# Kernel tuning notes

Measured on AMD Instinct MI355X. Metric: run time of the kernel, lower is better.

Reference implementation:

```python
import jax, jax.numpy as jnp
import numpy as np

SQ, SK, B, H, D = 2048, 2048, 2, 16, 64
LAYER_NUMBER = 1  # coeff for query_key_layer_scaling
MASK_FILL = -10000.0  # attention_mask_func fill value


def setup_inputs() -> dict:
    key = jax.random.key(0)
    kq, kk, kv = jax.random.split(key, 3)
    query_layer = jax.random.normal(kq, (SQ, B, H, D), dtype=jnp.float32)
    key_layer = jax.random.normal(kk, (SK, B, H, D), dtype=jnp.float32)
    value_layer = jax.random.normal(kv, (SK, B, H, D), dtype=jnp.float32)
    attention_mask = jnp.zeros((B, 1, SQ, SK), dtype=bool)  # ignored for causal mask type
    return {
        "query_layer": query_layer,
        "key_layer": key_layer,
        "value_layer": value_layer,
        "attention_mask": attention_mask,
    }


def reference(query_layer, key_layer, value_layer, attention_mask):
    sq, b, h, d = query_layer.shape
    sk = key_layer.shape[0]
    coeff = float(LAYER_NUMBER)
    norm_factor = np.sqrt(d) * coeff  # norm_factor = sqrt(d) * layer_number

    # BMM1: [b,h,sq,sk] scores, scaled by 1/norm_factor
    scores = jnp.einsum("sbhd,tbhd->bhst", query_layer, key_layer) / norm_factor

    # FusedScaleMaskSoftmax: scale by coeff in fp32, causal mask, softmax
    scores = scores.astype(jnp.float32) * coeff
    causal = jnp.triu(jnp.ones((sq, sk), dtype=bool), k=1)  # True above diagonal -> masked
    scores = jnp.where(causal[None, None], MASK_FILL, scores)
    probs = jax.nn.softmax(scores, axis=-1).astype(query_layer.dtype)

    # dropout p=0.0 -> identity

    # BMM2: context [sq,b,h,d] -> [sq,b,h*d]
    context = jnp.einsum("bhst,tbhd->sbhd", probs, value_layer)
    return context.reshape(sq, b, h * d)
```

## Files before the change

kernel.cpp:

```cpp
#include <hip/hip_runtime.h>

typedef short bf16x8 __attribute__((ext_vector_type(8)));
typedef float f32x4 __attribute__((ext_vector_type(4)));
typedef unsigned u32x4 __attribute__((ext_vector_type(4)));
typedef unsigned u32x2 __attribute__((ext_vector_type(2)));
typedef unsigned short ushort_t;

#define RS 2048
#define LDSK 72
#define QSCALE 0.18033688011f
#define BH_STRIDE (2048*64)

static __device__ __forceinline__ unsigned pkbf(float a, float b) {
    union { float f; unsigned u; } ua, ub; ua.f = a; ub.f = b;
    return ((ua.u + 0x8000u) >> 16) | ((ub.u + 0x8000u) & 0xffff0000u);
}

static __device__ __forceinline__ float fexp2(float x) {
#if __has_builtin(__builtin_amdgcn_exp2f)
    return __builtin_amdgcn_exp2f(x);
#else
    return exp2f(x);
#endif
}

__global__ __launch_bounds__(256)
void prep_bf16(const float* __restrict__ K, const float* __restrict__ V,
               ushort_t* __restrict__ Kbf, ushort_t* __restrict__ Vtb)
{
    __shared__ short Tt[64 * LDSK];
    const int kt = blockIdx.x, bh = blockIdx.y;
    const int t = threadIdx.x;
    {
        const int key = t >> 2, cq = (t & 3) * 16;
        const float* kp = K + (size_t)(kt * 64 + key) * RS + bh * 64 + cq;
        f32x4 a0 = *(const f32x4*)kp,       a1 = *(const f32x4*)(kp + 4);
        f32x4 a2 = *(const f32x4*)(kp + 8), a3 = *(const f32x4*)(kp + 12);
        u32x4 w0, w1;
        w0[0] = pkbf(a0[0], a0[1]); w0[1] = pkbf(a0[2], a0[3]);
        w0[2] = pkbf(a1[0], a1[1]); w0[3] = pkbf(a1[2], a1[3]);
        w1[0] = pkbf(a2[0], a2[1]); w1[1] = pkbf(a2[2], a2[3]);
        w1[2] = pkbf(a3[0], a3[1]); w1[3] = pkbf(a3[2], a3[3]);
        ushort_t* kout = Kbf + (size_t)bh * BH_STRIDE + (size_t)(kt * 64 + key) * 64 + cq;
        *(u32x4*)kout = w0;
        *(u32x4*)(kout + 8) = w1;
    }
    {
        const int vkey = (t & 31) * 2, vd = (t >> 5) * 8;
        const float* vp = V + (size_t)(kt * 64 + vkey) * RS + bh * 64 + vd;
        f32x4 b0 = *(const f32x4*)vp,        b1 = *(const f32x4*)(vp + 4);
        f32x4 c0 = *(const f32x4*)(vp + RS), c1 = *(const f32x4*)(vp + RS + 4);
        #pragma unroll
        for (int i = 0; i < 4; ++i) {
            *(unsigned*)&Tt[(vd + i) * LDSK + vkey]     = pkbf(b0[i], c0[i]);
            *(unsigned*)&Tt[(vd + 4 + i) * LDSK + vkey] = pkbf(b1[i], c1[i]);
        }
    }
    __syncthreads();
    {
        const int d = t >> 2, kq = (t & 3) * 16;
        ushort_t* vout = Vtb + (size_t)bh * BH_STRIDE + (size_t)d * RS + kt * 64 + kq;
        u32x4 w0 = *(const u32x4*)&Tt[d * LDSK + kq];
        u32x4 w1 = *(const u32x4*)&Tt[d * LDSK + kq + 8];
        *(u32x4*)vout = w0;
        *(u32x4*)(vout + 8) = w1;
    }
}

__global__ __launch_bounds__(128, 2)
void fa_fwd3(const float* __restrict__ Q, const ushort_t* __restrict__ Kbf,
             const ushort_t* __restrict__ Vtb, float* __restrict__ Out)
{
    __shared__ short Vt[64 * LDSK];
    __shared__ short Psh[2][32 * LDSK];

    const int x = blockIdx.x;
    const int chunk = x >> 8, idx = x & 255;
    const int bh = idx & 31, s = idx >> 5;
    const int qt = (chunk == 0) ? (31 - s) : (chunk == 1) ? (23 - s)
                 : (chunk == 2) ? s : (8 + s);
    const int base = bh * 64;
    const int tid = threadIdx.x;
    const int wave = tid >> 6, lane = tid & 63;
    const int n15 = lane & 15, quad = lane >> 4;
    const int q0 = qt * 64;
    const int qw = q0 + wave * 32;

    const ushort_t* Kb = Kbf + (size_t)bh * BH_STRIDE;

    const int r0 = tid >> 2, cc = (tid & 3) * 16;
    const ushort_t* vb = Vtb + (size_t)bh * BH_STRIDE + (size_t)r0 * RS + cc;

    bf16x8 qf[2][2];
    #pragma unroll
    for (int qg = 0; qg < 2; ++qg) {
        const float* qp = Q + (size_t)(qw + qg * 16 + n15) * RS + base + quad * 8;
        #pragma unroll
        for (int ks = 0; ks < 2; ++ks) {
            f32x4 a0 = *(const f32x4*)(qp + ks * 32) * QSCALE;
            f32x4 a1 = *(const f32x4*)(qp + ks * 32 + 4) * QSCALE;
            union { u32x4 u; bf16x8 s; } w;
            w.u[0] = pkbf(a0[0], a0[1]); w.u[1] = pkbf(a0[2], a0[3]);
            w.u[2] = pkbf(a1[0], a1[1]); w.u[3] = pkbf(a1[2], a1[3]);
            qf[qg][ks] = w.s;
        }
    }

    f32x4 O[2][4];
    #pragma unroll
    for (int qg = 0; qg < 2; ++qg)
        #pragma unroll
        for (int i = 0; i < 4; ++i) O[qg][i] = (f32x4){0.f, 0.f, 0.f, 0.f};
    float l[2] = {0.f, 0.f};

    u32x4 pv0, pv1, pv2, pv3;
    auto prefetchV = [&](int kt) {
        const ushort_t* vp = vb + kt * 64;
        pv0 = *(const u32x4*)vp;             pv1 = *(const u32x4*)(vp + 8);
        pv2 = *(const u32x4*)(vp + 32 * RS); pv3 = *(const u32x4*)(vp + 32 * RS + 8);
    };
    auto stageV = [&]() {
        *(u32x4*)&Vt[r0 * LDSK + cc] = pv0;
        *(u32x4*)&Vt[r0 * LDSK + cc + 8] = pv1;
        *(u32x4*)&Vt[(r0 + 32) * LDSK + cc] = pv2;
        *(u32x4*)&Vt[(r0 + 32) * LDSK + cc + 8] = pv3;
    };

    auto compute = [&](int kt) {
        const int kb = kt * 64;
        const ushort_t* kfp = Kb + (size_t)(kb + n15) * 64 + quad * 8;
        bf16x8 kf[4][2];
        #pragma unroll
        for (int mb = 0; mb < 4; ++mb) {
            kf[mb][0] = *(const bf16x8*)(kfp + mb * 16 * 64);
            kf[mb][1] = *(const bf16x8*)(kfp + mb * 16 * 64 + 32);
        }
        f32x4 S[2][4];
        #pragma unroll
        for (int mb = 0; mb < 4; ++mb)
            #pragma unroll
            for (int qg = 0; qg < 2; ++qg) {
                f32x4 sv = (f32x4){0.f, 0.f, 0.f, 0.f};
                sv = __builtin_amdgcn_mfma_f32_16x16x32_bf16(kf[mb][0], qf[qg][0], sv, 0, 0, 0);
                sv = __builtin_amdgcn_mfma_f32_16x16x32_bf16(kf[mb][1], qf[qg][1], sv, 0, 0, 0);
                S[qg][mb] = sv;
            }
        if (kt == qt) {
            #pragma unroll
            for (int qg = 0; qg < 2; ++qg) {
                int q = qw + qg * 16 + n15;
                #pragma unroll
                for (int mb = 0; mb < 4; ++mb)
                    #pragma unroll
                    for (int r = 0; r < 4; ++r)
                        if (kb + mb * 16 + quad * 4 + r > q) S[qg][mb][r] = -1e30f;
            }
        }
        #pragma unroll
        for (int qg = 0; qg < 2; ++qg) {
            float rs = 0.f;
            #pragma unroll
            for (int mb = 0; mb < 4; ++mb) {
                float p0 = fexp2(S[qg][mb][0]), p1 = fexp2(S[qg][mb][1]);
                float p2 = fexp2(S[qg][mb][2]), p3 = fexp2(S[qg][mb][3]);
                rs += (p0 + p1) + (p2 + p3);
                u32x2 w; w[0] = pkbf(p0, p1); w[1] = pkbf(p2, p3);
                *(u32x2*)&Psh[wave][(qg * 16 + n15) * LDSK + mb * 16 + quad * 4] = w;
            }
            rs += __shfl_xor(rs, 16);
            rs += __shfl_xor(rs, 32);
            l[qg] += rs;
        }
        bf16x8 pf[2][2];
        #pragma unroll
        for (int qg = 0; qg < 2; ++qg) {
            pf[qg][0] = *(const bf16x8*)&Psh[wave][(qg * 16 + n15) * LDSK + quad * 8];
            pf[qg][1] = *(const bf16x8*)&Psh[wave][(qg * 16 + n15) * LDSK + 32 + quad * 8];
        }
        #pragma unroll
        for (int db = 0; db < 4; ++db) {
            bf16x8 vf0 = *(const bf16x8*)&Vt[(db * 16 + n15) * LDSK + quad * 8];
            bf16x8 vf1 = *(const bf16x8*)&Vt[(db * 16 + n15) * LDSK + 32 + quad * 8];
            #pragma unroll
            for (int qg = 0; qg < 2; ++qg) {
                O[qg][db] = __builtin_amdgcn_mfma_f32_16x16x32_bf16(pf[qg][0], vf0, O[qg][db], 0, 0, 0);
                O[qg][db] = __builtin_amdgcn_mfma_f32_16x16x32_bf16(pf[qg][1], vf1, O[qg][db], 0, 0, 0);
            }
        }
    };

    prefetchV(0);
    for (int kt = 0; kt <= qt; ++kt) {
        __syncthreads();
        stageV();
        __syncthreads();
        if (kt < qt) prefetchV(kt + 1);
        compute(kt);
    }

    #pragma unroll
    for (int qg = 0; qg < 2; ++qg)
        #pragma unroll
        for (int r = 0; r < 4; ++r) {
            float inv = 1.0f / __shfl(l[qg], quad * 4 + r);
            size_t row = (size_t)(qw + qg * 16 + quad * 4 + r) * RS + base;
            #pragma unroll
            for (int db = 0; db < 4; ++db)
                Out[row + db * 16 + n15] = O[qg][db][r] * inv;
        }
}

__global__ __launch_bounds__(256, 3)
void fa_fwd_fb(const float* __restrict__ Q, const float* __restrict__ K,
               const float* __restrict__ V, float* __restrict__ Out)
{
    __shared__ short Ksh[2][64 * LDSK];
    __shared__ short Vt[2][64 * LDSK];
    __shared__ short Psh[4][16 * LDSK];

    const int qt = 31 - blockIdx.y;
    const int bh = blockIdx.x;
    const int base = bh * 64;
    const int tid = threadIdx.x;
    const int wave = tid >> 6, lane = tid & 63;
    const int n15 = lane & 15, quad = lane >> 4;
    const int q0 = qt * 64;
    const int krow = tid >> 2, kcg = (tid & 3) * 16;
    const int vkey = (tid & 31) * 2, vd = (tid >> 5) * 4;

    bf16x8 qf[2];
    {
        const float* qp = Q + (size_t)(q0 + wave * 16 + n15) * RS + base + quad * 8;
        #pragma unroll
        for (int ks = 0; ks < 2; ++ks) {
            f32x4 a0 = *(const f32x4*)(qp + ks * 32) * QSCALE;
            f32x4 a1 = *(const f32x4*)(qp + ks * 32 + 4) * QSCALE;
            union { u32x4 u; bf16x8 s; } w;
            w.u[0] = pkbf(a0[0], a0[1]); w.u[1] = pkbf(a0[2], a0[3]);
            w.u[2] = pkbf(a1[0], a1[1]); w.u[3] = pkbf(a1[2], a1[3]);
            qf[ks] = w.s;
        }
    }
    f32x4 O[4];
    #pragma unroll
    for (int i = 0; i < 4; ++i) O[i] = (f32x4){0.f, 0.f, 0.f, 0.f};
    float l = 0.f;
    f32x4 rk0, rk1, rk2, rk3, rv0, rv1, rv2, rv3;
    auto prefetch = [&](int kt) {
        const int kb = kt * 64;
        const float* kp = K + (size_t)(kb + krow) * RS + base + kcg;
        rk0 = *(const f32x4*)kp;       rk1 = *(const f32x4*)(kp + 4);
        rk2 = *(const f32x4*)(kp + 8); rk3 = *(const f32x4*)(kp + 12);
        const float* vp = V + (size_t)(kb + vkey) * RS + base + vd;
        rv0 = *(const f32x4*)vp;        rv1 = *(const f32x4*)(vp + RS);
        rv2 = *(const f32x4*)(vp + 32); rv3 = *(const f32x4*)(vp + RS + 32);
    };
    auto stage = [&](int buf) {
        u32x4 w0; w0[0] = pkbf(rk0[0], rk0[1]); w0[1] = pkbf(rk0[2], rk0[3]);
                  w0[2] = pkbf(rk1[0], rk1[1]); w0[3] = pkbf(rk1[2], rk1[3]);
        *(u32x4*)&Ksh[buf][krow * LDSK + kcg] = w0;
        u32x4 w1; w1[0] = pkbf(rk2[0], rk2[1]); w1[1] = pkbf(rk2[2], rk2[3]);
                  w1[2] = pkbf(rk3[0], rk3[1]); w1[3] = pkbf(rk3[2], rk3[3]);
        *(u32x4*)&Ksh[buf][krow * LDSK + kcg + 8] = w1;
        #pragma unroll
        for (int i = 0; i < 4; ++i) {
            *(unsigned*)&Vt[buf][(vd + i) * LDSK + vkey] = pkbf(rv0[i], rv1[i]);
            *(unsigned*)&Vt[buf][(vd + 32 + i) * LDSK + vkey] = pkbf(rv2[i], rv3[i]);
        }
    };
    auto compute = [&](int buf, int kb, bool diag) {
        f32x4 S[4];
        #pragma unroll
        for (int mb = 0; mb < 4; ++mb) {
            f32x4 sv = (f32x4){0.f, 0.f, 0.f, 0.f};
            bf16x8 kf0 = *(const bf16x8*)&Ksh[buf][(mb * 16 + n15) * LDSK + quad * 8];
            sv = __builtin_amdgcn_mfma_f32_16x16x32_bf16(kf0, qf[0], sv, 0, 0, 0);
            bf16x8 kf1 = *(const bf16x8*)&Ksh[buf][(mb * 16 + n15) * LDSK + 32 + quad * 8];
            sv = __builtin_amdgcn_mfma_f32_16x16x32_bf16(kf1, qf[1], sv, 0, 0, 0);
            S[mb] = sv;
        }
        if (diag) {
            int q = q0 + wave * 16 + n15;
            #pragma unroll
            for (int mb = 0; mb < 4; ++mb)
                #pragma unroll
                for (int r = 0; r < 4; ++r)
                    if (kb + mb * 16 + quad * 4 + r > q) S[mb][r] = -1e30f;
        }
        float rs = 0.f;
        #pragma unroll
        for (int mb = 0; mb < 4; ++mb) {
            float p0 = fexp2(S[mb][0]), p1 = fexp2(S[mb][1]);
            float p2 = fexp2(S[mb][2]), p3 = fexp2(S[mb][3]);
            rs += (p0 + p1) + (p2 + p3);
            u32x2 w; w[0] = pkbf(p0, p1); w[1] = pkbf(p2, p3);
            *(u32x2*)&Psh[wave][n15 * LDSK + mb * 16 + quad * 4] = w;
        }
        rs += __shfl_xor(rs, 16);
        rs += __shfl_xor(rs, 32);
        l += rs;
        bf16x8 pf0 = *(const bf16x8*)&Psh[wave][n15 * LDSK + quad * 8];
        bf16x8 pf1 = *(const bf16x8*)&Psh[wave][n15 * LDSK + 32 + quad * 8];
        #pragma unroll
        for (int db = 0; db < 4; ++db) {
            bf16x8 vf0 = *(const bf16x8*)&Vt[buf][(db * 16 + n15) * LDSK + quad * 8];
            O[db] = __builtin_amdgcn_mfma_f32_16x16x32_bf16(pf0, vf0, O[db], 0, 0, 0);
            bf16x8 vf1 = *(const bf16x8*)&Vt[buf][(db * 16 + n15) * LDSK + 32 + quad * 8];
            O[db] = __builtin_amdgcn_mfma_f32_16x16x32_bf16(pf1, vf1, O[db], 0, 0, 0);
        }
    };
    prefetch(0);
    stage(0);
    __syncthreads();
    for (int kt = 0; kt <= qt; ++kt) {
        const int cur = kt & 1;
        if (kt < qt) prefetch(kt + 1);
        compute(cur, kt * 64, kt == qt);
        if (kt < qt) stage(1 - cur);
        __syncthreads();
    }
    #pragma unroll
    for (int r = 0; r < 4; ++r) {
        float inv = 1.0f / __shfl(l, quad * 4 + r);
        size_t row = (size_t)(q0 + wave * 16 + quad * 4 + r) * RS + base;
        #pragma unroll
        for (int db = 0; db < 4; ++db)
            Out[row + db * 16 + n15] = O[db][r] * inv;
    }
}

extern "C" void kernel_launch(void* const* d_in, const int* in_sizes, int n_in,
                              void* d_out, int out_size, void* d_ws, size_t ws_size,
                              hipStream_t stream) {
    const float* Q = (const float*)d_in[0];
    const float* K = (const float*)d_in[1];
    const float* V = (const float*)d_in[2];
    float* Out = (float*)d_out;

    if (ws_size >= (size_t)2 * 32 * BH_STRIDE * sizeof(ushort_t)) {
        ushort_t* Kbf = (ushort_t*)d_ws;
        ushort_t* Vtb = Kbf + (size_t)32 * BH_STRIDE;
        prep_bf16<<<dim3(32, 32), dim3(256), 0, stream>>>(K, V, Kbf, Vtb);
        fa_fwd3<<<dim3(1024), dim3(128), 0, stream>>>(Q, Kbf, Vtb, Out);
    } else {
        fa_fwd_fb<<<dim3(32, 32), dim3(256), 0, stream>>>(Q, K, V, Out);
    }
}
```

Baseline: 158.5 us.

## Use 128-row query tiles with four waves sharing LDS-staged K and V

Each block now covers 128 query rows with four waves instead of 64 rows with two, so every K/V tile loaded is reused by twice as many query rows. K is also staged cooperatively into shared memory alongside V, replacing the per-wave global loads of K fragments. The grid drops to 512 blocks with a two-way pairing of heavy and light causal tiles. In exchange, LDS use per block rises, there are fewer blocks to balance across CUs, and in the diagonal tiles some waves sit idle while others compute.

```diff
diff --git a/kernel.cpp b/kernel.cpp
--- a/kernel.cpp
+++ b/kernel.cpp
@@ -67,29 +67,29 @@
     }
 }
 
-__global__ __launch_bounds__(128, 2)
-void fa_fwd3(const float* __restrict__ Q, const ushort_t* __restrict__ Kbf,
+__global__ __launch_bounds__(256, 2)
+void fa_fwd4(const float* __restrict__ Q, const ushort_t* __restrict__ Kbf,
              const ushort_t* __restrict__ Vtb, float* __restrict__ Out)
 {
+    __shared__ short Ksh[64 * LDSK];
     __shared__ short Vt[64 * LDSK];
-    __shared__ short Psh[2][32 * LDSK];
-
-    const int x = blockIdx.x;
-    const int chunk = x >> 8, idx = x & 255;
+    __shared__ short Psh[4][32 * LDSK];
+
+    const int bx = blockIdx.x;
+    const int chunk = bx >> 8, idx = bx & 255;
     const int bh = idx & 31, s = idx >> 5;
-    const int qt = (chunk == 0) ? (31 - s) : (chunk == 1) ? (23 - s)
-                 : (chunk == 2) ? s : (8 + s);
+    const int x = (chunk == 0) ? (15 - s) : s;
     const int base = bh * 64;
     const int tid = threadIdx.x;
     const int wave = tid >> 6, lane = tid & 63;
     const int n15 = lane & 15, quad = lane >> 4;
-    const int q0 = qt * 64;
+    const int q0 = x * 128;
     const int qw = q0 + wave * 32;
-
-    const ushort_t* Kb = Kbf + (size_t)bh * BH_STRIDE;
+    const int ktmax = 2 * x + 1;
 
     const int r0 = tid >> 2, cc = (tid & 3) * 16;
-    const ushort_t* vb = Vtb + (size_t)bh * BH_STRIDE + (size_t)r0 * RS + cc;
+    const ushort_t* kbp = Kbf + (size_t)bh * BH_STRIDE + r0 * 64 + cc;
+    const ushort_t* vbp = Vtb + (size_t)bh * BH_STRIDE + (size_t)r0 * RS + cc;
 
     bf16x8 qf[2][2];
     #pragma unroll
@@ -113,27 +113,29 @@
         for (int i = 0; i < 4; ++i) O[qg][i] = (f32x4){0.f, 0.f, 0.f, 0.f};
     float l[2] = {0.f, 0.f};
 
-    u32x4 pv0, pv1, pv2, pv3;
-    auto prefetchV = [&](int kt) {
-        const ushort_t* vp = vb + kt * 64;
-        pv0 = *(const u32x4*)vp;             pv1 = *(const u32x4*)(vp + 8);
-        pv2 = *(const u32x4*)(vp + 32 * RS); pv3 = *(const u32x4*)(vp + 32 * RS + 8);
-    };
-    auto stageV = [&]() {
+    u32x4 pk0, pk1, pv0, pv1;
+    auto prefetch = [&](int kt) {
+        const ushort_t* kp = kbp + (size_t)kt * 4096;
+        pk0 = *(const u32x4*)kp;
+        pk1 = *(const u32x4*)(kp + 8);
+        const ushort_t* vp = vbp + kt * 64;
+        pv0 = *(const u32x4*)vp;
+        pv1 = *(const u32x4*)(vp + 8);
+    };
+    auto stage = [&]() {
+        *(u32x4*)&Ksh[r0 * LDSK + cc] = pk0;
+        *(u32x4*)&Ksh[r0 * LDSK + cc + 8] = pk1;
         *(u32x4*)&Vt[r0 * LDSK + cc] = pv0;
         *(u32x4*)&Vt[r0 * LDSK + cc + 8] = pv1;
-        *(u32x4*)&Vt[(r0 + 32) * LDSK + cc] = pv2;
-        *(u32x4*)&Vt[(r0 + 32) * LDSK + cc + 8] = pv3;
     };
 
     auto compute = [&](int kt) {
         const int kb = kt * 64;
-        const ushort_t* kfp = Kb + (size_t)(kb + n15) * 64 + quad * 8;
         bf16x8 kf[4][2];
         #pragma unroll
         for (int mb = 0; mb < 4; ++mb) {
-            kf[mb][0] = *(const bf16x8*)(kfp + mb * 16 * 64);
-            kf[mb][1] = *(const bf16x8*)(kfp + mb * 16 * 64 + 32);
+            kf[mb][0] = *(const bf16x8*)&Ksh[(mb * 16 + n15) * LDSK + quad * 8];
+            kf[mb][1] = *(const bf16x8*)&Ksh[(mb * 16 + n15) * LDSK + 32 + quad * 8];
         }
         f32x4 S[2][4];
         #pragma unroll
@@ -145,7 +147,7 @@
                 sv = __builtin_amdgcn_mfma_f32_16x16x32_bf16(kf[mb][1], qf[qg][1], sv, 0, 0, 0);
                 S[qg][mb] = sv;
             }
-        if (kt == qt) {
+        if (kb + 63 > qw) {
             #pragma unroll
             for (int qg = 0; qg < 2; ++qg) {
                 int q = qw + qg * 16 + n15;
@@ -189,13 +191,14 @@
         }
     };
 
-    prefetchV(0);
-    for (int kt = 0; kt <= qt; ++kt) {
+    prefetch(0);
+    for (int kt = 0; kt <= ktmax; ++kt) {
         __syncthreads();
-        stageV();
+        stage();
         __syncthreads();
-        if (kt < qt) prefetchV(kt + 1);
-        compute(kt);
+        if (kt < ktmax) prefetch(kt + 1);
+        if (kt * 64 <= qw + 31)
+            compute(kt);
     }
 
     #pragma unroll
@@ -341,7 +344,7 @@
         ushort_t* Kbf = (ushort_t*)d_ws;
         ushort_t* Vtb = Kbf + (size_t)32 * BH_STRIDE;
         prep_bf16<<<dim3(32, 32), dim3(256), 0, stream>>>(K, V, Kbf, Vtb);
-        fa_fwd3<<<dim3(1024), dim3(128), 0, stream>>>(Q, Kbf, Vtb, Out);
+        fa_fwd4<<<dim3(512), dim3(256), 0, stream>>>(Q, Kbf, Vtb, Out);
     } else {
         fa_fwd_fb<<<dim3(32, 32), dim3(256), 0, stream>>>(Q, K, V, Out);
     }
```

Result: faster. 142.5 us (-10.1%).
